# Optimization experiments

Hardware: AMD Instinct MI355X
Metric: run time of the kernel (lower is better)

## Reference

```python
import jax, jax.numpy as jnp
import numpy as np

N = 100000       # nodes
E = 1600000      # edges (avg degree 16)
D_IN = 64
D_H = 64
D_OUT = 32
G = 64           # graphs in the batch


def setup_inputs() -> dict:
    key = jax.random.key(0)
    ks = jax.random.split(key, 10)
    x = jnp.zeros((N,), dtype=jnp.int32)  # embedding vocab is 1 -> all indices 0
    edge_index = jax.random.randint(ks[0], (2, E), 0, N, dtype=jnp.int32)
    batch = jnp.sort(jax.random.randint(ks[1], (N,), 0, G, dtype=jnp.int32))
    emb = jax.random.normal(ks[2], (1, D_IN), dtype=jnp.float32)
    W1 = jax.random.normal(ks[3], (D_IN, D_H), dtype=jnp.float32) * 0.05
    b1 = jax.random.normal(ks[4], (D_H,), dtype=jnp.float32) * 0.05
    W2 = jax.random.normal(ks[5], (D_H, D_H), dtype=jnp.float32) * 0.05
    b2 = jax.random.normal(ks[6], (D_H,), dtype=jnp.float32) * 0.05
    fcW = jax.random.normal(ks[7], (D_H, D_OUT), dtype=jnp.float32) * 0.05
    fcb = jax.random.normal(ks[8], (D_OUT,), dtype=jnp.float32) * 0.05
    return {"x": x, "edge_index": edge_index, "batch": batch, "emb": emb,
            "W1": W1, "b1": b1, "W2": W2, "b2": b2, "fcW": fcW, "fcb": fcb}


def _gcn_conv(h, W, b, src, dst):
    # PyG GCNConv with add_self_loops=True, symmetric normalization:
    # out = D^{-1/2} (A + I) D^{-1/2} (h @ W) + b, with deg computed on dst + self loop.
    h = h @ W  # [N, D]
    deg = jnp.zeros((N,), h.dtype).at[dst].add(1.0) + 1.0  # +1 for self loop
    dinv = jax.lax.rsqrt(deg)  # [N]
    norm = dinv[src] * dinv[dst]  # [E]
    agg = jax.ops.segment_sum(h[src] * norm[:, None], dst, num_segments=N)
    # self-loop term: norm_ii = dinv_i * dinv_i
    return agg + h * (dinv * dinv)[:, None] + b


def reference(x, edge_index, batch, emb, W1, b1, W2, b2, fcW, fcb):
    src, dst = edge_index[0], edge_index[1]
    h = emb[x]  # [N, D_IN] embedding lookup
    h = jax.nn.relu(_gcn_conv(h, W1, b1, src, dst))
    # dropout is identity in eval mode
    h = jax.nn.relu(_gcn_conv(h, W2, b2, src, dst))
    # global mean pool per graph
    sums = jax.ops.segment_sum(h, batch, num_segments=G)            # [G, D_H]
    cnt = jax.ops.segment_sum(jnp.ones((N,), h.dtype), batch, num_segments=G)
    pooled = sums / jnp.maximum(cnt, 1.0)[:, None]
    return pooled @ fcW + fcb  # [G, D_OUT]
```

## Files before the change

kernel.cpp:

```cpp
#include <hip/hip_runtime.h>
#include <hip/hip_bf16.h>


#define DH 64
#define DOUT 32
#define NBIN 65
#define BW 64
#define MAXNB 2048
#define SRCM 0x3FFFFFF
#define CAPE 1280
#define GPB 128
#define NSH 8

__global__ __launch_bounds__(1024) void k_group(
        const int* __restrict__ src, const int* __restrict__ dst,
        int* __restrict__ cursor, unsigned* __restrict__ rec,
        const float* __restrict__ emb, const float* __restrict__ W1,
        const float* __restrict__ b1, const float* __restrict__ W2,
        float* __restrict__ tarr, float2* __restrict__ PQ, int E, int NB, int chunk) {
    __shared__ int lh[MAXNB];
    __shared__ int lb[MAXNB];
    __shared__ float ewl[DH], tl[DH], bl[DH];
    __shared__ int rl[DH], sl[DH];
    int tid = threadIdx.x, bid = blockIdx.x;
    if (bid >= GPB) {
        int beta = bid - GPB;
        int k = tid;
        float s = 0.f, t = 0.f;
        if (k < DH) {
#pragma unroll
            for (int j = 0; j < DH; ++j) s += emb[j] * W1[j * DH + k];
            t = (s != 0.f) ? (-b1[k] / s) : INFINITY;
            ewl[k] = s; tl[k] = t; bl[k] = b1[k];
        }
        __syncthreads();
        if (k < DH) {
            int r = 0, ss = 0;
#pragma unroll
            for (int j = 0; j < DH; ++j) { r += (tl[j] <= t); ss += (tl[j] < t); }
            rl[k] = r; sl[k] = ss;
            if (beta == 0) tarr[k] = t;
        }
        __syncthreads();
        if (k < DH) {
            float p = 0.f, q = 0.f;
            for (int kk = 0; kk < DH; ++kk) {
                float e = ewl[kk];
                bool act;
                if (e > 0.f) act = (beta >= rl[kk]);
                else if (e < 0.f) act = (beta <= sl[kk]);
                else act = (bl[kk] > 0.f);
                if (act) {
                    float w = W2[kk * DH + k];
                    p += e * w;
                    q += bl[kk] * w;
                }
            }
            PQ[beta * DH + k] = make_float2(p, q);
        }
        return;
    }
    int c0 = bid * chunk;
    int c1 = min(c0 + chunk, E);
    for (int t = tid; t < NB; t += blockDim.x) lh[t] = 0;
    __syncthreads();
    for (int e = c0 + tid; e < c1; e += blockDim.x)
        atomicAdd(&lh[dst[e] >> 6], 1);
    __syncthreads();
    for (int t = tid; t < NB; t += blockDim.x) {
        int h = lh[t];
        lb[t] = h ? atomicAdd(&cursor[t], h) : 0;
    }
    __syncthreads();
    for (int t = tid; t < NB; t += blockDim.x) lh[t] = 0;
    __syncthreads();
    for (int e = c0 + tid; e < c1; e += blockDim.x) {
        int s = src[e], dd = dst[e];
        int bk = dd >> 6;
        int ofs = lb[bk] + atomicAdd(&lh[bk], 1);
        if (ofs < CAPE)
            rec[bk * CAPE + ofs] = (unsigned)s | ((unsigned)(dd & 63) << 26);
    }
}

__global__ __launch_bounds__(256) void k_passA(const int* __restrict__ cursor,
        const unsigned* __restrict__ rec, float* __restrict__ dinv, int N) {
    __shared__ int cl[BW];
    int tid = threadIdx.x;
    if (tid < BW) cl[tid] = 0;
    __syncthreads();
    int b = blockIdx.x;
    int cnt = min(cursor[b], CAPE);
    int r0 = b * CAPE;
    for (int e = tid; e < cnt; e += blockDim.x)
        atomicAdd(&cl[rec[r0 + e] >> 26], 1);
    __syncthreads();
    if (tid < BW) {
        int i = b * BW + tid;
        if (i < N) dinv[i] = rsqrtf((float)cl[tid] + 1.0f);
    }
}

__global__ __launch_bounds__(256, 8) void k_passB(const int* __restrict__ cursor,
        const unsigned* __restrict__ rec, const float* __restrict__ dinv,
        const float* __restrict__ tarr, float4* __restrict__ summary,
        int* __restrict__ flags, int N) {
    __shared__ float Sl[BW];
    __shared__ float tl[DH];
    int tid = threadIdx.x;
    if (tid < BW) Sl[tid] = 0.f;
    if (tid < DH) tl[tid] = tarr[tid];
    __syncthreads();
    int b = blockIdx.x;
    int cnt = min(cursor[b], CAPE);
    int r0 = b * CAPE;
    const uint4* rq = (const uint4*)(rec + r0);
    int nq = cnt >> 2;
    for (int q = tid; q < nq; q += blockDim.x) {
        uint4 r = rq[q];
        float d0 = dinv[r.x & SRCM];
        float d1 = dinv[r.y & SRCM];
        float d2 = dinv[r.z & SRCM];
        float d3 = dinv[r.w & SRCM];
        atomicAdd(&Sl[r.x >> 26], d0);
        atomicAdd(&Sl[r.y >> 26], d1);
        atomicAdd(&Sl[r.z >> 26], d2);
        atomicAdd(&Sl[r.w >> 26], d3);
    }
    int e = (nq << 2) + tid;
    if (e < cnt) {
        unsigned r = rec[r0 + e];
        atomicAdd(&Sl[r >> 26], dinv[r & SRCM]);
    }
    __syncthreads();
    if (tid < BW) {
        int i = b * BW + tid;
        if (i < N) {
            float di = dinv[i];
            float c = di * (Sl[tid] + di);
            int bb = 0;
#pragma unroll
            for (int j = 0; j < DH; ++j) bb += (tl[j] < c);
            summary[i] = make_float4(di * c, di, __uint_as_float((unsigned)bb), 0.f);
            flags[bb] = 1;
        }
    }
}

__global__ __launch_bounds__(256, 4) void k_passC(const int* __restrict__ cursor,
        const unsigned* __restrict__ rec, const float4* __restrict__ summary,
        const float2* __restrict__ PQ, const int* __restrict__ flags,
        const float* __restrict__ b2, const int* __restrict__ batch,
        float* __restrict__ psum_s, float* __restrict__ cnt_s, int N, int G) {
    __shared__ __align__(16) float AB[BW * NBIN * 2];
    __shared__ unsigned char ulist[NBIN + 3];
    __shared__ int UcntS;
    int tid = threadIdx.x;
    if (tid < 64) {
        int act = (flags[tid] != 0);
        unsigned long long m = __ballot(act);
        int pos = __popcll(m & ((1ull << tid) - 1ull));
        if (act) ulist[pos] = (unsigned char)tid;
        if (tid == 0) {
            int total = __popcll(m);
            if (flags[64]) ulist[total++] = 64;
            UcntS = total;
        }
    }
    float4* AB4 = (float4*)AB;
    for (int t = tid; t < (BW * NBIN * 2) / 4; t += blockDim.x)
        AB4[t] = make_float4(0.f, 0.f, 0.f, 0.f);
    __syncthreads();
    int b = blockIdx.x;
    int ecnt = min(cursor[b], CAPE);
    int r0 = b * CAPE;
    const uint4* rq = (const uint4*)(rec + r0);
    int nq = ecnt >> 2;
    for (int q = tid; q < nq; q += blockDim.x) {
        uint4 r = rq[q];
        float4 s0 = summary[r.x & SRCM];
        float4 s1 = summary[r.y & SRCM];
        float4 s2 = summary[r.z & SRCM];
        float4 s3 = summary[r.w & SRCM];
        float* p0 = &AB[(((r.x >> 26)) * NBIN + __float_as_uint(s0.z)) * 2];
        atomicAdd(p0, s0.x); atomicAdd(p0 + 1, s0.y);
        float* p1 = &AB[(((r.y >> 26)) * NBIN + __float_as_uint(s1.z)) * 2];
        atomicAdd(p1, s1.x); atomicAdd(p1 + 1, s1.y);
        float* p2 = &AB[(((r.z >> 26)) * NBIN + __float_as_uint(s2.z)) * 2];
        atomicAdd(p2, s2.x); atomicAdd(p2 + 1, s2.y);
        float* p3 = &AB[(((r.w >> 26)) * NBIN + __float_as_uint(s3.z)) * 2];
        atomicAdd(p3, s3.x); atomicAdd(p3 + 1, s3.y);
    }
    int e = (nq << 2) + tid;
    if (e < ecnt) {
        unsigned r = rec[r0 + e];
        float4 sm = summary[r & SRCM];
        float* pp = &AB[((r >> 26) * NBIN + __float_as_uint(sm.z)) * 2];
        atomicAdd(pp, sm.x); atomicAdd(pp + 1, sm.y);
    }
    __syncthreads();
    int U = UcntS;
    int d = tid & 63;
    int w = tid >> 6;
    int n0b = w << 4;
    float2 abr[16];
#pragma unroll
    for (int j = 0; j < 16; ++j)
        abr[j] = *(const float2*)&AB[((n0b + j) * NBIN + d) * 2];
    float accv[16];
#pragma unroll
    for (int j = 0; j < 16; ++j) accv[j] = 0.f;
    for (int uu = 0; uu < U; ++uu) {
        int u = ulist[uu];
        float2 pq = PQ[u * DH + d];
        if (u < 64) {
#pragma unroll
            for (int j = 0; j < 16; ++j) {
                float ax = __int_as_float(__builtin_amdgcn_readlane(__float_as_int(abr[j].x), u));
                float ay = __int_as_float(__builtin_amdgcn_readlane(__float_as_int(abr[j].y), u));
                accv[j] += ax * pq.x + ay * pq.y;
            }
        } else {
#pragma unroll
            for (int j = 0; j < 16; ++j) {
                float2 v = *(const float2*)&AB[((n0b + j) * NBIN + 64) * 2];
                accv[j] += v.x * pq.x + v.y * pq.y;
            }
        }
    }
    float* psum = psum_s + (size_t)(b & (NSH - 1)) * G * DH;
    float* cnt  = cnt_s  + (size_t)(b & (NSH - 1)) * G;
    int n0 = b * BW;
    float bias = b2[d];
    float lsum = 0.f, lcnt = 0.f;
    int cb = -1;
    for (int j = 0; j < 16; ++j) {
        int i = n0 + n0b + j;
        if (i >= N) break;
        float4 sm = summary[i];
        int rb = (int)__float_as_uint(sm.z);
        float2 pq = PQ[rb * DH + d];
        float g = sm.x * pq.x + sm.y * pq.y;
        float v = fmaxf(sm.y * (accv[j] + g) + bias, 0.f);
        int bt = batch[i];
        if (bt != cb) {
            if (cb >= 0) {
                atomicAdd(&psum[cb * DH + d], lsum);
                if (d == 0) atomicAdd(&cnt[cb], lcnt);
            }
            cb = bt; lsum = 0.f; lcnt = 0.f;
        }
        lsum += v;
        if (d == 0) lcnt += 1.f;
    }
    if (cb >= 0) {
        atomicAdd(&psum[cb * DH + d], lsum);
        if (d == 0) atomicAdd(&cnt[cb], lcnt);
    }
}

__global__ __launch_bounds__(64) void k_out(const float* __restrict__ psum_s,
        const float* __restrict__ cnt_s, const float* __restrict__ fcW,
        const float* __restrict__ fcb, float* __restrict__ out, int G) {
    __shared__ float pooled[DH];
    int g = blockIdx.x, d = threadIdx.x;
    float s = 0.f, cc = 0.f;
#pragma unroll
    for (int k = 0; k < NSH; ++k) {
        s += psum_s[(size_t)k * G * DH + g * DH + d];
        cc += cnt_s[(size_t)k * G + g];
    }
    pooled[d] = s / fmaxf(cc, 1.0f);
    __syncthreads();
    if (d < DOUT) {
        float o = 0.f;
#pragma unroll
        for (int kk = 0; kk < DH; ++kk) o += pooled[kk] * fcW[kk * DOUT + d];
        out[g * DOUT + d] = o + fcb[d];
    }
}

static inline size_t pad256(size_t n) { return (n + 255) & ~(size_t)255; }

extern "C" void kernel_launch(void* const* d_in, const int* in_sizes, int n_in,
                              void* d_out, int out_size, void* d_ws, size_t ws_size,
                              hipStream_t stream) {
    const int N = in_sizes[0];
    const int E = in_sizes[1] / 2;
    const int G = out_size / DOUT;
    const int NB = (N + BW - 1) / BW;

    const int* edge = (const int*)d_in[1];
    const int* src = edge;
    const int* dst = edge + E;
    const int* batch = (const int*)d_in[2];
    const float* emb = (const float*)d_in[3];
    const float* W1 = (const float*)d_in[4];
    const float* b1 = (const float*)d_in[5];
    const float* W2 = (const float*)d_in[6];
    const float* b2 = (const float*)d_in[7];
    const float* fcW = (const float*)d_in[8];
    const float* fcb = (const float*)d_in[9];
    float* out = (float*)d_out;

    char* ws = (char*)d_ws;
    size_t off = 0;
    float* psum_s = (float*)(ws + off); off += pad256((size_t)NSH * G * DH) * 4;
    float* cnt_s  = (float*)(ws + off); off += pad256((size_t)NSH * G) * 4;
    int* flags  = (int*)(ws + off);    off += pad256(NBIN) * 4;
    int* cursor = (int*)(ws + off);    off += pad256(MAXNB) * 4;
    size_t zero_bytes = off;
    unsigned* rec = (unsigned*)(ws + off); off += pad256((size_t)MAXNB * CAPE) * 4;
    float* dinv  = (float*)(ws + off);  off += pad256(N) * 4;
    float* tarr  = (float*)(ws + off);  off += pad256(DH) * 4;
    float2* PQ   = (float2*)(ws + off); off += pad256(NBIN * DH) * 8;
    float4* summary = (float4*)(ws + off); off += pad256(N) * 16;

    hipMemsetAsync(d_ws, 0, zero_bytes, stream);

    const int B = 256;
    int chunk = (E + GPB - 1) / GPB;
    k_group<<<GPB + NBIN, 1024, 0, stream>>>(src, dst, cursor, rec, emb, W1, b1, W2,
                                             tarr, PQ, E, NB, chunk);
    k_passA<<<NB, B, 0, stream>>>(cursor, rec, dinv, N);
    k_passB<<<NB, B, 0, stream>>>(cursor, rec, dinv, tarr, summary, flags, N);
    k_passC<<<NB, B, 0, stream>>>(cursor, rec, summary, PQ, flags, b2, batch,
                                  psum_s, cnt_s, N, G);
    k_out<<<G, 64, 0, stream>>>(psum_s, cnt_s, fcW, fcb, out, G);
}
```

Before: 156.7 us.

## Compact active bins in passC shared histogram and process in groups of 16

The passC kernel now remaps active bin ids to dense indices and keeps a shared accumulator of only 16 (+1 pad) bins per node instead of all 65. When more than 16 bins are active it loops, rescanning the edge list for each group of bins. The smaller shared footprint allows raising the occupancy hint from 4 to 6 blocks per CU. The cost is repeated edge gathers and atomics when many bins are active, plus extra barriers.

Measured after the change: 156.9 us. No clear change (+0.2%).

```diff
diff --git a/kernel.cpp b/kernel.cpp
--- a/kernel.cpp
+++ b/kernel.cpp
@@ -11,6 +11,8 @@
 #define CAPE 1280
 #define GPB 128
 #define NSH 8
+#define UMAX 16
+#define NST 17
 
 __global__ __launch_bounds__(1024) void k_group(
         const int* __restrict__ src, const int* __restrict__ dst,
@@ -147,86 +149,100 @@
     }
 }
 
-__global__ __launch_bounds__(256, 4) void k_passC(const int* __restrict__ cursor,
+__global__ __launch_bounds__(256, 6) void k_passC(const int* __restrict__ cursor,
         const unsigned* __restrict__ rec, const float4* __restrict__ summary,
         const float2* __restrict__ PQ, const int* __restrict__ flags,
         const float* __restrict__ b2, const int* __restrict__ batch,
         float* __restrict__ psum_s, float* __restrict__ cnt_s, int N, int G) {
-    __shared__ __align__(16) float AB[BW * NBIN * 2];
+    __shared__ __align__(16) float AB[BW * NST * 2];
     __shared__ unsigned char ulist[NBIN + 3];
+    __shared__ unsigned char bmap[NBIN + 3];
     __shared__ int UcntS;
     int tid = threadIdx.x;
     if (tid < 64) {
         int act = (flags[tid] != 0);
         unsigned long long m = __ballot(act);
         int pos = __popcll(m & ((1ull << tid) - 1ull));
-        if (act) ulist[pos] = (unsigned char)tid;
+        if (act) { ulist[pos] = (unsigned char)tid; bmap[tid] = (unsigned char)pos; }
         if (tid == 0) {
             int total = __popcll(m);
-            if (flags[64]) ulist[total++] = 64;
+            if (flags[64]) { ulist[total] = 64; bmap[64] = (unsigned char)total; total++; }
             UcntS = total;
         }
     }
-    float4* AB4 = (float4*)AB;
-    for (int t = tid; t < (BW * NBIN * 2) / 4; t += blockDim.x)
-        AB4[t] = make_float4(0.f, 0.f, 0.f, 0.f);
-    __syncthreads();
+    __syncthreads();
+    int U = UcntS;
     int b = blockIdx.x;
     int ecnt = min(cursor[b], CAPE);
     int r0 = b * CAPE;
     const uint4* rq = (const uint4*)(rec + r0);
     int nq = ecnt >> 2;
-    for (int q = tid; q < nq; q += blockDim.x) {
-        uint4 r = rq[q];
-        float4 s0 = summary[r.x & SRCM];
-        float4 s1 = summary[r.y & SRCM];
-        float4 s2 = summary[r.z & SRCM];
-        float4 s3 = summary[r.w & SRCM];
-        float* p0 = &AB[(((r.x >> 26)) * NBIN + __float_as_uint(s0.z)) * 2];
-        atomicAdd(p0, s0.x); atomicAdd(p0 + 1, s0.y);
-        float* p1 = &AB[(((r.y >> 26)) * NBIN + __float_as_uint(s1.z)) * 2];
-        atomicAdd(p1, s1.x); atomicAdd(p1 + 1, s1.y);
-        float* p2 = &AB[(((r.z >> 26)) * NBIN + __float_as_uint(s2.z)) * 2];
-        atomicAdd(p2, s2.x); atomicAdd(p2 + 1, s2.y);
-        float* p3 = &AB[(((r.w >> 26)) * NBIN + __float_as_uint(s3.z)) * 2];
-        atomicAdd(p3, s3.x); atomicAdd(p3 + 1, s3.y);
-    }
-    int e = (nq << 2) + tid;
-    if (e < ecnt) {
-        unsigned r = rec[r0 + e];
-        float4 sm = summary[r & SRCM];
-        float* pp = &AB[((r >> 26) * NBIN + __float_as_uint(sm.z)) * 2];
-        atomicAdd(pp, sm.x); atomicAdd(pp + 1, sm.y);
-    }
-    __syncthreads();
-    int U = UcntS;
     int d = tid & 63;
     int w = tid >> 6;
     int n0b = w << 4;
-    float2 abr[16];
-#pragma unroll
-    for (int j = 0; j < 16; ++j)
-        abr[j] = *(const float2*)&AB[((n0b + j) * NBIN + d) * 2];
     float accv[16];
 #pragma unroll
     for (int j = 0; j < 16; ++j) accv[j] = 0.f;
-    for (int uu = 0; uu < U; ++uu) {
-        int u = ulist[uu];
-        float2 pq = PQ[u * DH + d];
-        if (u < 64) {
+    for (int g0 = 0; g0 < U; g0 += UMAX) {
+        int gend = min(U, g0 + UMAX);
+        float4* AB4 = (float4*)AB;
+        for (int t = tid; t < (BW * NST * 2) / 4; t += 256)
+            AB4[t] = make_float4(0.f, 0.f, 0.f, 0.f);
+        __syncthreads();
+        for (int q = tid; q < nq; q += 256) {
+            uint4 r = rq[q];
+            float4 s0 = summary[r.x & SRCM];
+            float4 s1 = summary[r.y & SRCM];
+            float4 s2 = summary[r.z & SRCM];
+            float4 s3 = summary[r.w & SRCM];
+            int cb0 = (int)bmap[__float_as_uint(s0.z)] - g0;
+            int cb1 = (int)bmap[__float_as_uint(s1.z)] - g0;
+            int cb2 = (int)bmap[__float_as_uint(s2.z)] - g0;
+            int cb3 = (int)bmap[__float_as_uint(s3.z)] - g0;
+            if ((unsigned)cb0 < UMAX) {
+                float* p = &AB[((r.x >> 26) * NST + cb0) * 2];
+                atomicAdd(p, s0.x); atomicAdd(p + 1, s0.y);
+            }
+            if ((unsigned)cb1 < UMAX) {
+                float* p = &AB[((r.y >> 26) * NST + cb1) * 2];
+                atomicAdd(p, s1.x); atomicAdd(p + 1, s1.y);
+            }
+            if ((unsigned)cb2 < UMAX) {
+                float* p = &AB[((r.z >> 26) * NST + cb2) * 2];
+                atomicAdd(p, s2.x); atomicAdd(p + 1, s2.y);
+            }
+            if ((unsigned)cb3 < UMAX) {
+                float* p = &AB[((r.w >> 26) * NST + cb3) * 2];
+                atomicAdd(p, s3.x); atomicAdd(p + 1, s3.y);
+            }
+        }
+        int e = (nq << 2) + tid;
+        if (e < ecnt) {
+            unsigned r = rec[r0 + e];
+            float4 sm = summary[r & SRCM];
+            int cb = (int)bmap[__float_as_uint(sm.z)] - g0;
+            if ((unsigned)cb < UMAX) {
+                float* p = &AB[((r >> 26) * NST + cb) * 2];
+                atomicAdd(p, sm.x); atomicAdd(p + 1, sm.y);
+            }
+        }
+        __syncthreads();
+        float2 abr[16];
+#pragma unroll
+        for (int j = 0; j < 16; ++j)
+            abr[j] = *(const float2*)&AB[((n0b + j) * NST + (d & 15)) * 2];
+        for (int uu = g0; uu < gend; ++uu) {
+            int lane = uu - g0;
+            int u = ulist[uu];
+            float2 pq = PQ[u * DH + d];
 #pragma unroll
             for (int j = 0; j < 16; ++j) {
-                float ax = __int_as_float(__builtin_amdgcn_readlane(__float_as_int(abr[j].x), u));
-                float ay = __int_as_float(__builtin_amdgcn_readlane(__float_as_int(abr[j].y), u));
+                float ax = __int_as_float(__builtin_amdgcn_readlane(__float_as_int(abr[j].x), lane));
+                float ay = __int_as_float(__builtin_amdgcn_readlane(__float_as_int(abr[j].y), lane));
                 accv[j] += ax * pq.x + ay * pq.y;
             }
-        } else {
-#pragma unroll
-            for (int j = 0; j < 16; ++j) {
-                float2 v = *(const float2*)&AB[((n0b + j) * NBIN + 64) * 2];
-                accv[j] += v.x * pq.x + v.y * pq.y;
-            }
-        }
+        }
+        if (g0 + UMAX < U) __syncthreads();
     }
     float* psum = psum_s + (size_t)(b & (NSH - 1)) * G * DH;
     float* cnt  = cnt_s  + (size_t)(b & (NSH - 1)) * G;
```
